# Performance work log

Measured on AMD Instinct MI355X. Metric: run time of the kernel, lower is better.

Reference implementation:

```python
import jax, jax.numpy as jnp
import numpy as np

L = 32768      # sequence length
D_MODEL = 256  # input/output feature dim
D_HIDDEN = 256 # diagonal recurrent state dim
R_MIN, R_MAX, MAX_PHASE = 0.0, 1.0, 6.28


def setup_inputs() -> dict:
    key = jax.random.key(0)
    ks = jax.random.split(key, 8)
    inputs = jax.random.normal(ks[0], (L, D_MODEL), dtype=jnp.float32)
    # nu_init: log(-0.5*log(u*(r_max^2-r_min^2)+r_min^2))
    u1 = jax.random.uniform(ks[1], (D_HIDDEN,), dtype=jnp.float32)
    nu_log = jnp.log(-0.5 * jnp.log(u1 * (R_MAX**2 - R_MIN**2) + R_MIN**2))
    # theta_init: log(max_phase*u)
    u2 = jax.random.uniform(ks[2], (D_HIDDEN,), dtype=jnp.float32)
    theta_log = jnp.log(MAX_PHASE * u2)
    # gamma_log_init from (nu_log, theta_log)
    diag_lambda = jnp.exp(-jnp.exp(nu_log) + 1j * jnp.exp(theta_log))
    gamma_log = jnp.log(jnp.sqrt(1.0 - jnp.abs(diag_lambda) ** 2))
    bnorm = np.sqrt(2 * D_MODEL).astype(np.float32) if False else jnp.sqrt(2.0 * D_MODEL)
    cnorm = jnp.sqrt(2.0 * D_HIDDEN)
    B_re = jax.random.normal(ks[3], (D_HIDDEN, D_MODEL), dtype=jnp.float32) / bnorm
    B_im = jax.random.normal(ks[4], (D_HIDDEN, D_MODEL), dtype=jnp.float32) / bnorm
    C_re = jax.random.normal(ks[5], (D_MODEL, D_HIDDEN), dtype=jnp.float32) / cnorm
    C_im = jax.random.normal(ks[6], (D_MODEL, D_HIDDEN), dtype=jnp.float32) / cnorm
    D = jax.random.normal(ks[7], (D_MODEL,), dtype=jnp.float32)
    return {"inputs": inputs, "nu_log": nu_log, "theta_log": theta_log,
            "gamma_log": gamma_log, "B_re": B_re, "B_im": B_im,
            "C_re": C_re, "C_im": C_im, "D": D}


def _binop(q_i, q_j):
    # elementwise diagonal linear-recurrence combine
    A_i, b_i = q_i
    A_j, b_j = q_j
    return (A_j * A_i, A_j * b_i + b_j)


def reference(inputs, nu_log, theta_log, gamma_log, B_re, B_im, C_re, C_im, D):
    # h_{t+1} = lambda * h_t + B_norm x_{t+1};  y_t = Re[C h_t] + D * x_t
    diag_lambda = jnp.exp(-jnp.exp(nu_log) + 1j * jnp.exp(theta_log))  # (H,)
    B_norm = (B_re + 1j * B_im) * jnp.exp(gamma_log)[:, None]          # (H, M)
    C = C_re + 1j * C_im                                               # (M, H)
    Bu = inputs.astype(B_norm.dtype) @ B_norm.T                        # (L, H) complex
    Lam = jnp.broadcast_to(diag_lambda, (inputs.shape[0], diag_lambda.shape[0]))
    _, h = jax.lax.associative_scan(_binop, (Lam, Bu))                 # (L, H)
    return jnp.real(h @ C.T) + inputs * D                              # (L, M)
```

## Files before the change

### kernel.cpp

```cpp
#include <hip/hip_runtime.h>
#include <hip/hip_bf16.h>
#include <math.h>

#define LSEQ 32768
#define DMODEL 256
#define DHID 256
#define NCH 512
#define CHUNK 128
#define NCHUNKS (LSEQ / CHUNK)

typedef __bf16 bf16_t;
typedef _Float16 f16_t;
typedef __bf16 bf16x8 __attribute__((ext_vector_type(8)));
typedef __bf16 bf16x4 __attribute__((ext_vector_type(4)));
typedef float f32x4 __attribute__((ext_vector_type(4)));

__device__ __forceinline__ void async_load16(const void* g, void* l) {
  __builtin_amdgcn_global_load_lds((__attribute__((address_space(1))) void*)g,
                                   (__attribute__((address_space(3))) void*)l,
                                   16, 0, 0);
}

__device__ __forceinline__ float f16tof(unsigned int u) {
  return (float)__builtin_bit_cast(_Float16, (unsigned short)(u & 0xffffu));
}
__device__ __forceinline__ unsigned short fTobf(float f) {
  return __builtin_bit_cast(unsigned short, (bf16_t)f);
}

__global__ void prep_params(const float* __restrict__ nu_log,
                            const float* __restrict__ theta_log,
                            float* __restrict__ lam ) {
  int h = threadIdx.x;
  if (h < DHID) {
    double nu = exp((double)nu_log[h]);
    double th = exp((double)theta_log[h]);
    double mag = exp(-nu);
    lam[h]            = (float)(mag * cos(th));
    lam[DHID + h]     = (float)(mag * sin(th));
    double magC = exp(-(double)CHUNK * nu);
    double phC  = fmod((double)CHUNK * th, 6.283185307179586);
    lam[2 * DHID + h] = (float)(magC * cos(phC));
    lam[3 * DHID + h] = (float)(magC * sin(phC));
    double mag32 = exp(-32.0 * nu);
    double ph32  = fmod(32.0 * th, 6.283185307179586);
    lam[4 * DHID + h] = (float)(mag32 * cos(ph32));
    lam[5 * DHID + h] = (float)(mag32 * sin(ph32));
  }
}

__global__ void pack_w1(const float* __restrict__ B_re, const float* __restrict__ B_im,
                        const float* __restrict__ gamma_log, bf16_t* __restrict__ W1) {
  int n = blockIdx.x, k = threadIdx.x;
  int h = n >> 1;
  float g = expf(gamma_log[h]);
  float v = (((n & 1) == 0) ? B_re[h * DMODEL + k] : B_im[h * DMODEL + k]) * g;
  W1[n * DMODEL + k] = (bf16_t)v;
}

__global__ void pack_w2(const float* __restrict__ C_re, const float* __restrict__ C_im,
                        bf16_t* __restrict__ W2) {
  int m = blockIdx.x, k = threadIdx.x;
  int h = k >> 1;
  float v = ((k & 1) == 0) ? C_re[m * DHID + h] : -C_im[m * DHID + h];
  W2[m * NCH + k] = (bf16_t)v;
}

__global__ void convert_x(const float* __restrict__ x, bf16_t* __restrict__ xb) {
  int i = blockIdx.x * 256 + threadIdx.x;
  float4 v = ((const float4*)x)[i];
  bf16x4 o = {(bf16_t)v.x, (bf16_t)v.y, (bf16_t)v.z, (bf16_t)v.w};
  ((bf16x4*)xb)[i] = o;
}

__global__ __launch_bounds__(512) void gemm1_scan(
    const bf16_t* __restrict__ A, const bf16_t* __restrict__ Bw,
    f16_t* __restrict__ Bu, const float* __restrict__ lam,
    float* __restrict__ E) {
  __shared__ __align__(16) char smem[69632];
  bf16_t* As = (bf16_t*)smem;
  bf16_t* Bs = (bf16_t*)(smem + 8192);
  char*   Bt = smem;
  float*  Ep = (float*)(smem + 65536);

  const int tid = threadIdx.x;
  const int gx = blockIdx.x;
  const int c  = blockIdx.y;
  const int r0 = c * CHUNK;
  const int c0 = gx * 256;
  const int wave = tid >> 6, lane = tid & 63;
  const int wm = wave & 1, wn = wave >> 1;
  const int lrow = lane & 15, lk = lane >> 4;
  const int ra = tid >> 2, ka = (tid & 3) * 8;

  f32x4 acc[4][4] = {};

  for (int k0 = 0; k0 < DMODEL; k0 += 32) {
    __syncthreads();
    async_load16(A + (size_t)(r0 + ra) * DMODEL + k0 + ka, (char*)As + tid * 16);
    async_load16(Bw + (size_t)(c0 + ra) * DMODEL + k0 + ka, (char*)Bs + tid * 16);
    async_load16(Bw + (size_t)(c0 + 128 + ra) * DMODEL + k0 + ka,
                 (char*)Bs + 8192 + tid * 16);
    __syncthreads();
    bf16x8 af[4], bfr[4];
#pragma unroll
    for (int i = 0; i < 4; ++i)
      af[i] = *(const bf16x8*)(As + (wm * 64 + i * 16 + lrow) * 32 + lk * 8);
#pragma unroll
    for (int j = 0; j < 4; ++j)
      bfr[j] = *(const bf16x8*)(Bs + (wn * 64 + j * 16 + lrow) * 32 + lk * 8);
#pragma unroll
    for (int i = 0; i < 4; ++i)
#pragma unroll
      for (int j = 0; j < 4; ++j)
        acc[i][j] = __builtin_amdgcn_mfma_f32_16x16x32_bf16(af[i], bfr[j], acc[i][j], 0, 0, 0);
  }
  __syncthreads();

#pragma unroll
  for (int i = 0; i < 4; ++i)
#pragma unroll
    for (int r = 0; r < 4; ++r) {
      int row = wm * 64 + i * 16 + lk * 4 + r;
      int key = (row & 7) << 4;
#pragma unroll
      for (int j = 0; j < 4; ++j) {
        int col = wn * 64 + j * 16 + lrow;
        *(f16_t*)(Bt + row * 512 + ((col * 2) ^ key)) = (f16_t)acc[i][j][r];
      }
    }
  __syncthreads();

  char* dst = (char*)Bu + (size_t)r0 * 1024 + gx * 512;
#pragma unroll
  for (int it = 0; it < 8; ++it) {
    int idx = it * 512 + tid;
    int row = idx >> 5, off = (idx & 31) * 16;
    *(f32x4*)(dst + (size_t)row * 1024 + off) = *(const f32x4*)(Bt + row * 512 + off);
  }

  {
    int p = tid & 127, seg = tid >> 7;
    int h = gx * 128 + p;
    float lre = lam[h], lim = lam[DHID + h];
    float sre = 0.f, sim = 0.f;
    int cb = 4 * p;
#pragma unroll 4
    for (int t = 0; t < 32; ++t) {
      int row = seg * 32 + t;
      unsigned int w = *(const unsigned int*)(Bt + row * 512 + (cb ^ ((row & 7) << 4)));
      float bre = f16tof(w), bim = f16tof(w >> 16);
      float nre = fmaf(lre, sre, fmaf(-lim, sim, bre));
      float nim = fmaf(lre, sim, fmaf(lim, sre, bim));
      sre = nre; sim = nim;
    }
    Ep[seg * 256 + 2 * p]     = sre;
    Ep[seg * 256 + 2 * p + 1] = sim;
  }
  __syncthreads();
  if (tid < 128) {
    int p = tid, h = gx * 128 + p;
    float ar = lam[4 * DHID + h], ai = lam[5 * DHID + h];
    float er = Ep[2 * p], ei = Ep[2 * p + 1];
#pragma unroll
    for (int s = 1; s < 4; ++s) {
      float tr = fmaf(ar, er, fmaf(-ai, ei, Ep[s * 256 + 2 * p]));
      float ti = fmaf(ar, ei, fmaf(ai, er, Ep[s * 256 + 2 * p + 1]));
      er = tr; ei = ti;
    }
    E[c * NCH + h]       = er;
    E[c * NCH + 256 + h] = ei;
  }
}

__global__ void scan_pass2(const float* __restrict__ E, const float* __restrict__ lam,
                           float* __restrict__ Sc) {
  int h = blockIdx.x, c = threadIdx.x;
  __shared__ float Ar[NCHUNKS], Ai[NCHUNKS], br[NCHUNKS], bi[NCHUNKS];
  float aR = lam[2 * DHID + h], aI = lam[3 * DHID + h];
  float bR = E[c * NCH + h], bI = E[c * NCH + 256 + h];
  Ar[c] = aR; Ai[c] = aI; br[c] = bR; bi[c] = bI;
  __syncthreads();
  for (int off = 1; off < NCHUNKS; off <<= 1) {
    float paR = 0, paI = 0, pbR = 0, pbI = 0;
    bool has = (c >= off);
    if (has) { paR = Ar[c - off]; paI = Ai[c - off]; pbR = br[c - off]; pbI = bi[c - off]; }
    __syncthreads();
    if (has) {
      float nAR = aR * paR - aI * paI;
      float nAI = aR * paI + aI * paR;
      float nbR = aR * pbR - aI * pbI + bR;
      float nbI = aR * pbI + aI * pbR + bI;
      aR = nAR; aI = nAI; bR = nbR; bI = nbI;
      Ar[c] = aR; Ai[c] = aI; br[c] = bR; bi[c] = bI;
    }
    __syncthreads();
  }
  float inR = (c > 0) ? br[c - 1] : 0.f;
  float inI = (c > 0) ? bi[c - 1] : 0.f;
  Sc[c * NCH + h]       = inR;
  Sc[c * NCH + 256 + h] = inI;
}

__global__ __launch_bounds__(512) void scan_gemm2(
    const f16_t* __restrict__ Bu, const bf16_t* __restrict__ W2,
    const float* __restrict__ lam, const float* __restrict__ Sc,
    const float* __restrict__ X, const float* __restrict__ Dv,
    float* __restrict__ out) {
  __shared__ __align__(16) char smem[147456];
  char*   H  = smem;
  bf16_t* Bs = (bf16_t*)(smem + 131072);
  const int tid = threadIdx.x;
  const int c = blockIdx.x;
  const int wave = tid >> 6, lane = tid & 63;
  const int wm = wave & 1, wn = wave >> 1;
  const int lrow = lane & 15, lk = lane >> 4;
  const int ra = tid >> 2, ka = (tid & 3) * 8;

  const char* src = (const char*)Bu + (size_t)c * CHUNK * 1024;
#pragma unroll
  for (int it = 0; it < 16; ++it)
    async_load16(src + it * 8192 + tid * 16, H + it * 8192 + tid * 16);
  __syncthreads();

  if (tid < 256) {
    int h = tid;
    float lre = lam[h], lim = lam[DHID + h];
    float sre = Sc[c * NCH + h], sim = Sc[c * NCH + 256 + h];
    int cb = 4 * h;
#pragma unroll 4
    for (int t = 0; t < CHUNK; ++t) {
      unsigned int* p = (unsigned int*)(H + t * 1024 + (cb ^ ((t & 7) << 4)));
      unsigned int w = *p;
      float bre = f16tof(w), bim = f16tof(w >> 16);
      float nre = fmaf(lre, sre, fmaf(-lim, sim, bre));
      float nim = fmaf(lre, sim, fmaf(lim, sre, bim));
      sre = nre; sim = nim;
      *p = ((unsigned int)fTobf(sim) << 16) | (unsigned int)fTobf(sre);
    }
  }

  f32x4 acc[4][4] = {};
  for (int k0 = 0; k0 < NCH; k0 += 32) {
    __syncthreads();
    async_load16(W2 + (size_t)ra * NCH + k0 + ka, (char*)Bs + tid * 16);
    async_load16(W2 + (size_t)(128 + ra) * NCH + k0 + ka, (char*)Bs + 8192 + tid * 16);
    __syncthreads();
    bf16x8 af[4], bfr[4];
#pragma unroll
    for (int i = 0; i < 4; ++i) {
      int m = wm * 64 + i * 16 + lrow;
      af[i] = *(const bf16x8*)(H + m * 1024 + ((2 * k0 + lk * 16) ^ ((m & 7) << 4)));
    }
#pragma unroll
    for (int j = 0; j < 4; ++j)
      bfr[j] = *(const bf16x8*)(Bs + (wn * 64 + j * 16 + lrow) * 32 + lk * 8);
#pragma unroll
    for (int i = 0; i < 4; ++i)
#pragma unroll
      for (int j = 0; j < 4; ++j)
        acc[i][j] = __builtin_amdgcn_mfma_f32_16x16x32_bf16(af[i], bfr[j], acc[i][j], 0, 0, 0);
  }

#pragma unroll
  for (int i = 0; i < 4; ++i)
#pragma unroll
    for (int r = 0; r < 4; ++r) {
      int row = c * CHUNK + wm * 64 + i * 16 + lk * 4 + r;
#pragma unroll
      for (int j = 0; j < 4; ++j) {
        int col = wn * 64 + j * 16 + lrow;
        float v = acc[i][j][r] + X[(size_t)row * DMODEL + col] * Dv[col];
        out[(size_t)row * DMODEL + col] = v;
      }
    }
}

extern "C" void kernel_launch(void* const* d_in, const int* in_sizes, int n_in,
                              void* d_out, int out_size, void* d_ws, size_t ws_size,
                              hipStream_t stream) {
  const float* inputs    = (const float*)d_in[0];
  const float* nu_log    = (const float*)d_in[1];
  const float* theta_log = (const float*)d_in[2];
  const float* gamma_log = (const float*)d_in[3];
  const float* B_re      = (const float*)d_in[4];
  const float* B_im      = (const float*)d_in[5];
  const float* C_re      = (const float*)d_in[6];
  const float* C_im      = (const float*)d_in[7];
  const float* Dvec      = (const float*)d_in[8];
  float* out = (float*)d_out;

  char* w = (char*)d_ws;
  bf16_t* W1 = (bf16_t*)w; w += (size_t)NCH * DMODEL * 2;
  bf16_t* W2 = (bf16_t*)w; w += (size_t)DMODEL * NCH * 2;
  float* lam = (float*)w;  w += 8192;
  bf16_t* xb = (bf16_t*)w; w += (size_t)LSEQ * DMODEL * 2;
  f16_t* Bu  = (f16_t*)w;  w += (size_t)LSEQ * NCH * 2;
  float* E   = (float*)w;  w += (size_t)NCHUNKS * NCH * 4;
  float* Sc  = (float*)w;  w += (size_t)NCHUNKS * NCH * 4;

  prep_params<<<1, 256, 0, stream>>>(nu_log, theta_log, lam);
  pack_w1<<<NCH, DMODEL, 0, stream>>>(B_re, B_im, gamma_log, W1);
  pack_w2<<<DMODEL, NCH, 0, stream>>>(C_re, C_im, W2);
  convert_x<<<(LSEQ * DMODEL) / 4 / 256, 256, 0, stream>>>(inputs, xb);

  gemm1_scan<<<dim3(2, NCHUNKS), 512, 0, stream>>>(xb, W1, Bu, lam, E);
  scan_pass2<<<DHID, NCHUNKS, 0, stream>>>(E, lam, Sc);
  scan_gemm2<<<NCHUNKS, 512, 0, stream>>>(Bu, W2, lam, Sc, inputs, Dvec, out);
}
```

Baseline: 165.7 us.

## Fuse GEMM1, chunk scan and GEMM2 into one cooperative kernel with grid sync

Merges the three main kernels into a single cooperative kernel with one block per chunk. The Bu tile stays in shared memory between GEMM1 and GEMM2, which removes the global Bu round trip and the separate scan_pass2 launch. After a grid-wide sync, each block computes its incoming carry serially from the per-chunk end states, combining two halves with precomputed powers of lambda. The costs are serial carry loops of up to 256 steps per block, a grid barrier, and a large shared-memory footprint that needs all 256 blocks to be co-resident.

```diff
diff --git a/kernel.cpp b/kernel.cpp
--- a/kernel.cpp
+++ b/kernel.cpp
@@ -1,4 +1,5 @@
 #include <hip/hip_runtime.h>
+#include <hip/hip_cooperative_groups.h>
 #include <hip/hip_bf16.h>
 #include <math.h>
 
@@ -9,6 +10,8 @@
 #define CHUNK 128
 #define NCHUNKS (LSEQ / CHUNK)
 
+namespace cg = cooperative_groups;
+
 typedef __bf16 bf16_t;
 typedef _Float16 f16_t;
 typedef __bf16 bf16x8 __attribute__((ext_vector_type(8)));
@@ -24,29 +27,27 @@
 __device__ __forceinline__ float f16tof(unsigned int u) {
   return (float)__builtin_bit_cast(_Float16, (unsigned short)(u & 0xffffu));
 }
-__device__ __forceinline__ unsigned short fTobf(float f) {
-  return __builtin_bit_cast(unsigned short, (bf16_t)f);
+__device__ __forceinline__ unsigned int fTobf(float f) {
+  return (unsigned int)__builtin_bit_cast(unsigned short, (bf16_t)f);
 }
 
 __global__ void prep_params(const float* __restrict__ nu_log,
                             const float* __restrict__ theta_log,
-                            float* __restrict__ lam ) {
+                            float* __restrict__ lam) {
   int h = threadIdx.x;
-  if (h < DHID) {
-    double nu = exp((double)nu_log[h]);
-    double th = exp((double)theta_log[h]);
-    double mag = exp(-nu);
-    lam[h]            = (float)(mag * cos(th));
-    lam[DHID + h]     = (float)(mag * sin(th));
-    double magC = exp(-(double)CHUNK * nu);
-    double phC  = fmod((double)CHUNK * th, 6.283185307179586);
-    lam[2 * DHID + h] = (float)(magC * cos(phC));
-    lam[3 * DHID + h] = (float)(magC * sin(phC));
-    double mag32 = exp(-32.0 * nu);
-    double ph32  = fmod(32.0 * th, 6.283185307179586);
-    lam[4 * DHID + h] = (float)(mag32 * cos(ph32));
-    lam[5 * DHID + h] = (float)(mag32 * sin(ph32));
-  }
+  if (h >= DHID) return;
+  double nu = exp((double)nu_log[h]);
+  double th = exp((double)theta_log[h]);
+#define PUT(row, n) { \
+    double mag = exp(-(double)(n) * nu); \
+    double ph  = fmod((double)(n) * th, 6.283185307179586); \
+    lam[(row) * DHID + h]     = (float)(mag * cos(ph)); \
+    lam[((row)+1) * DHID + h] = (float)(mag * sin(ph)); }
+  PUT(0, 1.0)
+  PUT(2, 128.0)
+  PUT(4, 64.0)
+  for (int j = 0; j < 8; ++j) PUT(6 + 2 * j, 128.0 * (double)(1 << j))
+#undef PUT
 }
 
 __global__ void pack_w1(const float* __restrict__ B_re, const float* __restrict__ B_im,
@@ -73,46 +74,51 @@
   ((bf16x4*)xb)[i] = o;
 }
 
-__global__ __launch_bounds__(512) void gemm1_scan(
-    const bf16_t* __restrict__ A, const bf16_t* __restrict__ Bw,
-    f16_t* __restrict__ Bu, const float* __restrict__ lam,
-    float* __restrict__ E) {
-  __shared__ __align__(16) char smem[69632];
-  bf16_t* As = (bf16_t*)smem;
-  bf16_t* Bs = (bf16_t*)(smem + 8192);
-  char*   Bt = smem;
-  float*  Ep = (float*)(smem + 65536);
+__global__ __launch_bounds__(512, 2) void lru_fused(
+    const bf16_t* __restrict__ A,
+    const bf16_t* __restrict__ W1,
+    const bf16_t* __restrict__ W2,
+    const float* __restrict__ lam,
+    float* __restrict__ E,
+    const float* __restrict__ X, const float* __restrict__ Dv,
+    float* __restrict__ out) {
+  __shared__ __align__(16) char smem[151552];
+  char*   H   = smem;
+  bf16_t* As  = (bf16_t*)smem;
+  bf16_t* Bs  = (bf16_t*)(smem + 8192);
+  bf16_t* Bs2 = (bf16_t*)(smem + 131072);
+  float*  Ep  = (float*)(smem + 147456);
 
   const int tid = threadIdx.x;
-  const int gx = blockIdx.x;
-  const int c  = blockIdx.y;
+  const int c = blockIdx.x;
   const int r0 = c * CHUNK;
-  const int c0 = gx * 256;
   const int wave = tid >> 6, lane = tid & 63;
   const int wm = wave & 1, wn = wave >> 1;
   const int lrow = lane & 15, lk = lane >> 4;
-  const int ra = tid >> 2, ka = (tid & 3) * 8;
-
-  f32x4 acc[4][4] = {};
-
+
+  f32x4 acc[4][8] = {};
   for (int k0 = 0; k0 < DMODEL; k0 += 32) {
     __syncthreads();
-    async_load16(A + (size_t)(r0 + ra) * DMODEL + k0 + ka, (char*)As + tid * 16);
-    async_load16(Bw + (size_t)(c0 + ra) * DMODEL + k0 + ka, (char*)Bs + tid * 16);
-    async_load16(Bw + (size_t)(c0 + 128 + ra) * DMODEL + k0 + ka,
-                 (char*)Bs + 8192 + tid * 16);
-    __syncthreads();
-    bf16x8 af[4], bfr[4];
+    async_load16(A + (size_t)(r0 + (tid >> 2)) * DMODEL + k0 + (tid & 3) * 8,
+                 (char*)As + tid * 16);
+#pragma unroll
+    for (int it = 0; it < 4; ++it) {
+      int idx = it * 512 + tid;
+      async_load16(W1 + (size_t)(idx >> 2) * DMODEL + k0 + (idx & 3) * 8,
+                   (char*)Bs + idx * 16);
+    }
+    __syncthreads();
+    bf16x8 af[4], bfr[8];
 #pragma unroll
     for (int i = 0; i < 4; ++i)
       af[i] = *(const bf16x8*)(As + (wm * 64 + i * 16 + lrow) * 32 + lk * 8);
 #pragma unroll
-    for (int j = 0; j < 4; ++j)
-      bfr[j] = *(const bf16x8*)(Bs + (wn * 64 + j * 16 + lrow) * 32 + lk * 8);
+    for (int j = 0; j < 8; ++j)
+      bfr[j] = *(const bf16x8*)(Bs + (wn * 128 + j * 16 + lrow) * 32 + lk * 8);
 #pragma unroll
     for (int i = 0; i < 4; ++i)
 #pragma unroll
-      for (int j = 0; j < 4; ++j)
+      for (int j = 0; j < 8; ++j)
         acc[i][j] = __builtin_amdgcn_mfma_f32_16x16x32_bf16(af[i], bfr[j], acc[i][j], 0, 0, 0);
   }
   __syncthreads();
@@ -124,153 +130,135 @@
       int row = wm * 64 + i * 16 + lk * 4 + r;
       int key = (row & 7) << 4;
 #pragma unroll
-      for (int j = 0; j < 4; ++j) {
-        int col = wn * 64 + j * 16 + lrow;
-        *(f16_t*)(Bt + row * 512 + ((col * 2) ^ key)) = (f16_t)acc[i][j][r];
+      for (int j = 0; j < 8; ++j) {
+        int col = wn * 128 + j * 16 + lrow;
+        *(f16_t*)(H + row * 1024 + ((col * 2) ^ key)) = (f16_t)acc[i][j][r];
       }
     }
   __syncthreads();
 
-  char* dst = (char*)Bu + (size_t)r0 * 1024 + gx * 512;
-#pragma unroll
-  for (int it = 0; it < 8; ++it) {
-    int idx = it * 512 + tid;
-    int row = idx >> 5, off = (idx & 31) * 16;
-    *(f32x4*)(dst + (size_t)row * 1024 + off) = *(const f32x4*)(Bt + row * 512 + off);
-  }
-
   {
-    int p = tid & 127, seg = tid >> 7;
-    int h = gx * 128 + p;
-    float lre = lam[h], lim = lam[DHID + h];
+    int p = tid & 255, seg = tid >> 8;
+    float lre = lam[p], lim = lam[DHID + p];
     float sre = 0.f, sim = 0.f;
     int cb = 4 * p;
 #pragma unroll 4
-    for (int t = 0; t < 32; ++t) {
-      int row = seg * 32 + t;
-      unsigned int w = *(const unsigned int*)(Bt + row * 512 + (cb ^ ((row & 7) << 4)));
+    for (int t = 0; t < 64; ++t) {
+      int row = seg * 64 + t;
+      unsigned int w = *(const unsigned int*)(H + row * 1024 + (cb ^ ((row & 7) << 4)));
       float bre = f16tof(w), bim = f16tof(w >> 16);
       float nre = fmaf(lre, sre, fmaf(-lim, sim, bre));
       float nim = fmaf(lre, sim, fmaf(lim, sre, bim));
       sre = nre; sim = nim;
     }
-    Ep[seg * 256 + 2 * p]     = sre;
-    Ep[seg * 256 + 2 * p + 1] = sim;
-  }
-  __syncthreads();
-  if (tid < 128) {
-    int p = tid, h = gx * 128 + p;
-    float ar = lam[4 * DHID + h], ai = lam[5 * DHID + h];
-    float er = Ep[2 * p], ei = Ep[2 * p + 1];
-#pragma unroll
-    for (int s = 1; s < 4; ++s) {
-      float tr = fmaf(ar, er, fmaf(-ai, ei, Ep[s * 256 + 2 * p]));
-      float ti = fmaf(ar, ei, fmaf(ai, er, Ep[s * 256 + 2 * p + 1]));
-      er = tr; ei = ti;
-    }
-    E[c * NCH + h]       = er;
-    E[c * NCH + 256 + h] = ei;
-  }
-}
-
-__global__ void scan_pass2(const float* __restrict__ E, const float* __restrict__ lam,
-                           float* __restrict__ Sc) {
-  int h = blockIdx.x, c = threadIdx.x;
-  __shared__ float Ar[NCHUNKS], Ai[NCHUNKS], br[NCHUNKS], bi[NCHUNKS];
-  float aR = lam[2 * DHID + h], aI = lam[3 * DHID + h];
-  float bR = E[c * NCH + h], bI = E[c * NCH + 256 + h];
-  Ar[c] = aR; Ai[c] = aI; br[c] = bR; bi[c] = bI;
-  __syncthreads();
-  for (int off = 1; off < NCHUNKS; off <<= 1) {
-    float paR = 0, paI = 0, pbR = 0, pbI = 0;
-    bool has = (c >= off);
-    if (has) { paR = Ar[c - off]; paI = Ai[c - off]; pbR = br[c - off]; pbI = bi[c - off]; }
-    __syncthreads();
-    if (has) {
-      float nAR = aR * paR - aI * paI;
-      float nAI = aR * paI + aI * paR;
-      float nbR = aR * pbR - aI * pbI + bR;
-      float nbI = aR * pbI + aI * pbR + bI;
-      aR = nAR; aI = nAI; bR = nbR; bI = nbI;
-      Ar[c] = aR; Ai[c] = aI; br[c] = bR; bi[c] = bI;
-    }
-    __syncthreads();
-  }
-  float inR = (c > 0) ? br[c - 1] : 0.f;
-  float inI = (c > 0) ? bi[c - 1] : 0.f;
-  Sc[c * NCH + h]       = inR;
-  Sc[c * NCH + 256 + h] = inI;
-}
-
-__global__ __launch_bounds__(512) void scan_gemm2(
-    const f16_t* __restrict__ Bu, const bf16_t* __restrict__ W2,
-    const float* __restrict__ lam, const float* __restrict__ Sc,
-    const float* __restrict__ X, const float* __restrict__ Dv,
-    float* __restrict__ out) {
-  __shared__ __align__(16) char smem[147456];
-  char*   H  = smem;
-  bf16_t* Bs = (bf16_t*)(smem + 131072);
-  const int tid = threadIdx.x;
-  const int c = blockIdx.x;
-  const int wave = tid >> 6, lane = tid & 63;
-  const int wm = wave & 1, wn = wave >> 1;
-  const int lrow = lane & 15, lk = lane >> 4;
-  const int ra = tid >> 2, ka = (tid & 3) * 8;
-
-  const char* src = (const char*)Bu + (size_t)c * CHUNK * 1024;
-#pragma unroll
-  for (int it = 0; it < 16; ++it)
-    async_load16(src + it * 8192 + tid * 16, H + it * 8192 + tid * 16);
-  __syncthreads();
-
+    Ep[seg * 512 + 2 * p]     = sre;
+    Ep[seg * 512 + 2 * p + 1] = sim;
+  }
+  __syncthreads();
   if (tid < 256) {
-    int h = tid;
-    float lre = lam[h], lim = lam[DHID + h];
-    float sre = Sc[c * NCH + h], sim = Sc[c * NCH + 256 + h];
-    int cb = 4 * h;
+    int p = tid;
+    float ar = lam[4 * DHID + p], ai = lam[5 * DHID + p];
+    float s0r = Ep[2 * p], s0i = Ep[2 * p + 1];
+    float s1r = Ep[512 + 2 * p], s1i = Ep[512 + 2 * p + 1];
+    float er = fmaf(ar, s0r, fmaf(-ai, s0i, s1r));
+    float ei = fmaf(ar, s0i, fmaf(ai, s0r, s1i));
+    E[(size_t)c * NCH + 2 * p]     = er;
+    E[(size_t)c * NCH + 2 * p + 1] = ei;
+  }
+  __threadfence();
+  cg::this_grid().sync();
+  __threadfence();
+
+  float carR = 0.f, carI = 0.f;
+  {
+    int p = tid & 255, hi = tid >> 8;
+    int half = c >> 1;
+    int lo = hi ? half : 0;
+    int hiEnd = hi ? c : half;
+    float aR = lam[2 * DHID + p], aI = lam[3 * DHID + p];
+    float sr = 0.f, si = 0.f;
+#pragma unroll 4
+    for (int k = lo; k < hiEnd; ++k) {
+      float2 e = *(const float2*)(E + (size_t)k * NCH + 2 * p);
+      float nr = fmaf(aR, sr, fmaf(-aI, si, e.x));
+      float ni = fmaf(aR, si, fmaf(aI, sr, e.y));
+      sr = nr; si = ni;
+    }
+    Ep[hi * 512 + 2 * p]     = sr;
+    Ep[hi * 512 + 2 * p + 1] = si;
+  }
+  __syncthreads();
+  if (tid < 256) {
+    int p = tid;
+    int lenb = c - (c >> 1);
+    float pr = 1.f, pi = 0.f;
+#pragma unroll
+    for (int j = 0; j < 8; ++j)
+      if (lenb & (1 << j)) {
+        float br = lam[(6 + 2 * j) * DHID + p], bi = lam[(7 + 2 * j) * DHID + p];
+        float nr = pr * br - pi * bi;
+        float ni = pr * bi + pi * br;
+        pr = nr; pi = ni;
+      }
+    float sar = Ep[2 * p], sai = Ep[2 * p + 1];
+    float sbr = Ep[512 + 2 * p], sbi = Ep[512 + 2 * p + 1];
+    carR = fmaf(pr, sar, fmaf(-pi, sai, sbr));
+    carI = fmaf(pr, sai, fmaf(pi, sar, sbi));
+  }
+  __syncthreads();
+
+  if (tid < 256) {
+    int p = tid;
+    float lre = lam[p], lim = lam[DHID + p];
+    float sre = carR, sim = carI;
+    int cb = 4 * p;
 #pragma unroll 4
     for (int t = 0; t < CHUNK; ++t) {
-      unsigned int* p = (unsigned int*)(H + t * 1024 + (cb ^ ((t & 7) << 4)));
-      unsigned int w = *p;
+      unsigned int* ptr = (unsigned int*)(H + t * 1024 + (cb ^ ((t & 7) << 4)));
+      unsigned int w = *ptr;
       float bre = f16tof(w), bim = f16tof(w >> 16);
       float nre = fmaf(lre, sre, fmaf(-lim, sim, bre));
       float nim = fmaf(lre, sim, fmaf(lim, sre, bim));
       sre = nre; sim = nim;
-      *p = ((unsigned int)fTobf(sim) << 16) | (unsigned int)fTobf(sre);
-    }
-  }
-
-  f32x4 acc[4][4] = {};
+      *ptr = (fTobf(sim) << 16) | fTobf(sre);
+    }
+  }
+
+  f32x4 acc2[4][4] = {};
   for (int k0 = 0; k0 < NCH; k0 += 32) {
     __syncthreads();
-    async_load16(W2 + (size_t)ra * NCH + k0 + ka, (char*)Bs + tid * 16);
-    async_load16(W2 + (size_t)(128 + ra) * NCH + k0 + ka, (char*)Bs + 8192 + tid * 16);
-    __syncthreads();
-    bf16x8 af[4], bfr[4];
+#pragma unroll
+    for (int it = 0; it < 2; ++it) {
+      int idx = it * 512 + tid;
+      async_load16(W2 + (size_t)(idx >> 2) * NCH + k0 + (idx & 3) * 8,
+                   (char*)Bs2 + idx * 16);
+    }
+    __syncthreads();
+    bf16x8 af2[4], bf2[4];
 #pragma unroll
     for (int i = 0; i < 4; ++i) {
       int m = wm * 64 + i * 16 + lrow;
-      af[i] = *(const bf16x8*)(H + m * 1024 + ((2 * k0 + lk * 16) ^ ((m & 7) << 4)));
+      af2[i] = *(const bf16x8*)(H + m * 1024 + ((2 * k0 + lk * 16) ^ ((m & 7) << 4)));
     }
 #pragma unroll
     for (int j = 0; j < 4; ++j)
-      bfr[j] = *(const bf16x8*)(Bs + (wn * 64 + j * 16 + lrow) * 32 + lk * 8);
+      bf2[j] = *(const bf16x8*)(Bs2 + (wn * 64 + j * 16 + lrow) * 32 + lk * 8);
 #pragma unroll
     for (int i = 0; i < 4; ++i)
 #pragma unroll
       for (int j = 0; j < 4; ++j)
-        acc[i][j] = __builtin_amdgcn_mfma_f32_16x16x32_bf16(af[i], bfr[j], acc[i][j], 0, 0, 0);
+        acc2[i][j] = __builtin_amdgcn_mfma_f32_16x16x32_bf16(af2[i], bf2[j], acc2[i][j], 0, 0, 0);
   }
 
 #pragma unroll
   for (int i = 0; i < 4; ++i)
 #pragma unroll
     for (int r = 0; r < 4; ++r) {
-      int row = c * CHUNK + wm * 64 + i * 16 + lk * 4 + r;
+      int row = r0 + wm * 64 + i * 16 + lk * 4 + r;
 #pragma unroll
       for (int j = 0; j < 4; ++j) {
         int col = wn * 64 + j * 16 + lrow;
-        float v = acc[i][j][r] + X[(size_t)row * DMODEL + col] * Dv[col];
+        float v = acc2[i][j][r] + X[(size_t)row * DMODEL + col] * Dv[col];
         out[(size_t)row * DMODEL + col] = v;
       }
     }
@@ -293,18 +281,16 @@
   char* w = (char*)d_ws;
   bf16_t* W1 = (bf16_t*)w; w += (size_t)NCH * DMODEL * 2;
   bf16_t* W2 = (bf16_t*)w; w += (size_t)DMODEL * NCH * 2;
-  float* lam = (float*)w;  w += 8192;
+  float* lam = (float*)w;  w += 24576;
   bf16_t* xb = (bf16_t*)w; w += (size_t)LSEQ * DMODEL * 2;
-  f16_t* Bu  = (f16_t*)w;  w += (size_t)LSEQ * NCH * 2;
   float* E   = (float*)w;  w += (size_t)NCHUNKS * NCH * 4;
-  float* Sc  = (float*)w;  w += (size_t)NCHUNKS * NCH * 4;
 
   prep_params<<<1, 256, 0, stream>>>(nu_log, theta_log, lam);
   pack_w1<<<NCH, DMODEL, 0, stream>>>(B_re, B_im, gamma_log, W1);
   pack_w2<<<DMODEL, NCH, 0, stream>>>(C_re, C_im, W2);
   convert_x<<<(LSEQ * DMODEL) / 4 / 256, 256, 0, stream>>>(inputs, xb);
 
-  gemm1_scan<<<dim3(2, NCHUNKS), 512, 0, stream>>>(xb, W1, Bu, lam, E);
-  scan_pass2<<<DHID, NCHUNKS, 0, stream>>>(E, lam, Sc);
-  scan_gemm2<<<NCHUNKS, 512, 0, stream>>>(Bu, W2, lam, Sc, inputs, Dvec, out);
-}
+  void* args[] = {&xb, &W1, &W2, &lam, &E, &inputs, &Dvec, &out};
+  hipLaunchCooperativeKernel((const void*)lru_fused, dim3(NCHUNKS), dim3(512),
+                             args, 0, stream);
+}
```

New measurement: 290.5 us. +75.3%, slower.

## Fuse prep kernels and fold cross-chunk carry scan into scan_gemm2

Applied to the files above, without the earlier changes.

Merges the four preprocessing kernels into one launch. It also drops the separate scan_pass2 kernel: each scan_gemm2 block now recomputes its own incoming state by sequentially combining all previous chunk end-states, split into two halves that are joined with precomputed powers of lambda. Blocks are issued in reverse chunk order to balance the O(c) carry loop. This removes two launches and an intermediate buffer, at the cost of redundant quadratic work over chunk summaries (up to 256 serial steps per block).

```diff
diff --git a/kernel.cpp b/kernel.cpp
--- a/kernel.cpp
+++ b/kernel.cpp
@@ -24,53 +24,50 @@
 __device__ __forceinline__ float f16tof(unsigned int u) {
   return (float)__builtin_bit_cast(_Float16, (unsigned short)(u & 0xffffu));
 }
-__device__ __forceinline__ unsigned short fTobf(float f) {
-  return __builtin_bit_cast(unsigned short, (bf16_t)f);
-}
-
-__global__ void prep_params(const float* __restrict__ nu_log,
-                            const float* __restrict__ theta_log,
-                            float* __restrict__ lam ) {
-  int h = threadIdx.x;
-  if (h < DHID) {
-    double nu = exp((double)nu_log[h]);
-    double th = exp((double)theta_log[h]);
-    double mag = exp(-nu);
-    lam[h]            = (float)(mag * cos(th));
-    lam[DHID + h]     = (float)(mag * sin(th));
-    double magC = exp(-(double)CHUNK * nu);
-    double phC  = fmod((double)CHUNK * th, 6.283185307179586);
-    lam[2 * DHID + h] = (float)(magC * cos(phC));
-    lam[3 * DHID + h] = (float)(magC * sin(phC));
-    double mag32 = exp(-32.0 * nu);
-    double ph32  = fmod(32.0 * th, 6.283185307179586);
-    lam[4 * DHID + h] = (float)(mag32 * cos(ph32));
-    lam[5 * DHID + h] = (float)(mag32 * sin(ph32));
-  }
-}
-
-__global__ void pack_w1(const float* __restrict__ B_re, const float* __restrict__ B_im,
-                        const float* __restrict__ gamma_log, bf16_t* __restrict__ W1) {
-  int n = blockIdx.x, k = threadIdx.x;
-  int h = n >> 1;
-  float g = expf(gamma_log[h]);
-  float v = (((n & 1) == 0) ? B_re[h * DMODEL + k] : B_im[h * DMODEL + k]) * g;
-  W1[n * DMODEL + k] = (bf16_t)v;
-}
-
-__global__ void pack_w2(const float* __restrict__ C_re, const float* __restrict__ C_im,
-                        bf16_t* __restrict__ W2) {
-  int m = blockIdx.x, k = threadIdx.x;
-  int h = k >> 1;
-  float v = ((k & 1) == 0) ? C_re[m * DHID + h] : -C_im[m * DHID + h];
-  W2[m * NCH + k] = (bf16_t)v;
-}
-
-__global__ void convert_x(const float* __restrict__ x, bf16_t* __restrict__ xb) {
-  int i = blockIdx.x * 256 + threadIdx.x;
-  float4 v = ((const float4*)x)[i];
-  bf16x4 o = {(bf16_t)v.x, (bf16_t)v.y, (bf16_t)v.z, (bf16_t)v.w};
-  ((bf16x4*)xb)[i] = o;
+__device__ __forceinline__ unsigned int fTobf(float f) {
+  return (unsigned int)__builtin_bit_cast(unsigned short, (bf16_t)f);
+}
+
+__global__ void prep_all(const float* __restrict__ nu_log,
+                         const float* __restrict__ theta_log,
+                         const float* __restrict__ gamma_log,
+                         const float* __restrict__ B_re, const float* __restrict__ B_im,
+                         const float* __restrict__ C_re, const float* __restrict__ C_im,
+                         const float* __restrict__ x,
+                         float* __restrict__ lam, bf16_t* __restrict__ W1,
+                         bf16_t* __restrict__ W2, bf16_t* __restrict__ xb) {
+  const int bid = blockIdx.x, tid = threadIdx.x;
+  if (bid == 0) {
+    int h = tid;
+    if (h < DHID) {
+      double nu = exp((double)nu_log[h]);
+      double th = exp((double)theta_log[h]);
+#define PUT(row, n) { \
+      double mag = exp(-(double)(n) * nu); \
+      double ph  = fmod((double)(n) * th, 6.283185307179586); \
+      lam[(row) * DHID + h]     = (float)(mag * cos(ph)); \
+      lam[((row)+1) * DHID + h] = (float)(mag * sin(ph)); }
+      PUT(0, 1.0)
+      PUT(2, 32.0)
+      for (int j = 0; j < 8; ++j) PUT(4 + 2 * j, 128.0 * (double)(1 << j))
+#undef PUT
+    }
+  } else if (bid < 513) {
+    int n = bid - 1, k = tid, h = n >> 1;
+    float g = expf(gamma_log[h]);
+    float v = (((n & 1) == 0) ? B_re[h * DMODEL + k] : B_im[h * DMODEL + k]) * g;
+    W1[n * DMODEL + k] = (bf16_t)v;
+  } else if (bid < 1025) {
+    int idx = bid - 513;
+    int m = idx >> 1, k = (idx & 1) * 256 + tid, h = k >> 1;
+    float v = ((k & 1) == 0) ? C_re[m * DHID + h] : -C_im[m * DHID + h];
+    W2[m * NCH + k] = (bf16_t)v;
+  } else {
+    int i = (bid - 1025) * 256 + tid;
+    float4 v = ((const float4*)x)[i];
+    bf16x4 o = {(bf16_t)v.x, (bf16_t)v.y, (bf16_t)v.z, (bf16_t)v.w};
+    ((bf16x4*)xb)[i] = o;
+  }
 }
 
 __global__ __launch_bounds__(512) void gemm1_scan(
@@ -160,7 +157,7 @@
   __syncthreads();
   if (tid < 128) {
     int p = tid, h = gx * 128 + p;
-    float ar = lam[4 * DHID + h], ai = lam[5 * DHID + h];
+    float ar = lam[2 * DHID + h], ai = lam[3 * DHID + h];
     float er = Ep[2 * p], ei = Ep[2 * p + 1];
 #pragma unroll
     for (int s = 1; s < 4; ++s) {
@@ -168,83 +165,92 @@
       float ti = fmaf(ar, ei, fmaf(ai, er, Ep[s * 256 + 2 * p + 1]));
       er = tr; ei = ti;
     }
-    E[c * NCH + h]       = er;
-    E[c * NCH + 256 + h] = ei;
-  }
-}
-
-__global__ void scan_pass2(const float* __restrict__ E, const float* __restrict__ lam,
-                           float* __restrict__ Sc) {
-  int h = blockIdx.x, c = threadIdx.x;
-  __shared__ float Ar[NCHUNKS], Ai[NCHUNKS], br[NCHUNKS], bi[NCHUNKS];
-  float aR = lam[2 * DHID + h], aI = lam[3 * DHID + h];
-  float bR = E[c * NCH + h], bI = E[c * NCH + 256 + h];
-  Ar[c] = aR; Ai[c] = aI; br[c] = bR; bi[c] = bI;
-  __syncthreads();
-  for (int off = 1; off < NCHUNKS; off <<= 1) {
-    float paR = 0, paI = 0, pbR = 0, pbI = 0;
-    bool has = (c >= off);
-    if (has) { paR = Ar[c - off]; paI = Ai[c - off]; pbR = br[c - off]; pbI = bi[c - off]; }
-    __syncthreads();
-    if (has) {
-      float nAR = aR * paR - aI * paI;
-      float nAI = aR * paI + aI * paR;
-      float nbR = aR * pbR - aI * pbI + bR;
-      float nbI = aR * pbI + aI * pbR + bI;
-      aR = nAR; aI = nAI; bR = nbR; bI = nbI;
-      Ar[c] = aR; Ai[c] = aI; br[c] = bR; bi[c] = bI;
-    }
-    __syncthreads();
-  }
-  float inR = (c > 0) ? br[c - 1] : 0.f;
-  float inI = (c > 0) ? bi[c - 1] : 0.f;
-  Sc[c * NCH + h]       = inR;
-  Sc[c * NCH + 256 + h] = inI;
+    E[(size_t)c * NCH + 2 * h]     = er;
+    E[(size_t)c * NCH + 2 * h + 1] = ei;
+  }
 }
 
 __global__ __launch_bounds__(512) void scan_gemm2(
     const f16_t* __restrict__ Bu, const bf16_t* __restrict__ W2,
-    const float* __restrict__ lam, const float* __restrict__ Sc,
+    const float* __restrict__ lam, const float* __restrict__ E,
     const float* __restrict__ X, const float* __restrict__ Dv,
     float* __restrict__ out) {
   __shared__ __align__(16) char smem[147456];
   char*   H  = smem;
   bf16_t* Bs = (bf16_t*)(smem + 131072);
+  float*  Ep = (float*)(smem + 131072);
+
   const int tid = threadIdx.x;
-  const int c = blockIdx.x;
+  const int c = (int)gridDim.x - 1 - (int)blockIdx.x;
+  const int r0 = c * CHUNK;
+
+  const char* src = (const char*)Bu + (size_t)r0 * 1024;
+#pragma unroll
+  for (int it = 0; it < 16; ++it)
+    async_load16(src + it * 8192 + tid * 16, H + it * 8192 + tid * 16);
+
+  {
+    int p = tid & 255, half = tid >> 8;
+    int m = c >> 1;
+    int lo = half ? m : 0, end = half ? c : m;
+    float aR = lam[4 * DHID + p], aI = lam[5 * DHID + p];
+    float sr = 0.f, si = 0.f;
+#pragma unroll 4
+    for (int k = lo; k < end; ++k) {
+      float2 e = *(const float2*)(E + (size_t)k * NCH + 2 * p);
+      float nr = fmaf(aR, sr, fmaf(-aI, si, e.x));
+      float ni = fmaf(aR, si, fmaf(aI, sr, e.y));
+      sr = nr; si = ni;
+    }
+    Ep[half * 512 + 2 * p]     = sr;
+    Ep[half * 512 + 2 * p + 1] = si;
+  }
+  __syncthreads();
+
+  if (tid < 256) {
+    int p = tid;
+    int lenb = c - (c >> 1);
+    float pr = 1.f, pi = 0.f;
+#pragma unroll
+    for (int j = 0; j < 8; ++j)
+      if (lenb & (1 << j)) {
+        float br = lam[(4 + 2 * j) * DHID + p], bi = lam[(5 + 2 * j) * DHID + p];
+        float nr = pr * br - pi * bi, ni = pr * bi + pi * br;
+        pr = nr; pi = ni;
+      }
+    float sar = Ep[2 * p], sai = Ep[2 * p + 1];
+    float sbr = Ep[512 + 2 * p], sbi = Ep[512 + 2 * p + 1];
+    float carR = fmaf(pr, sar, fmaf(-pi, sai, sbr));
+    float carI = fmaf(pr, sai, fmaf(pi, sar, sbi));
+
+    float lre = lam[p], lim = lam[DHID + p];
+    float sre = carR, sim = carI;
+    int cb = 4 * p;
+#pragma unroll 4
+    for (int t = 0; t < CHUNK; ++t) {
+      unsigned int* ptr = (unsigned int*)(H + t * 1024 + (cb ^ ((t & 7) << 4)));
+      unsigned int w = *ptr;
+      float bre = f16tof(w), bim = f16tof(w >> 16);
+      float nre = fmaf(lre, sre, fmaf(-lim, sim, bre));
+      float nim = fmaf(lre, sim, fmaf(lim, sre, bim));
+      sre = nre; sim = nim;
+      *ptr = (fTobf(sim) << 16) | fTobf(sre);
+    }
+  }
+
   const int wave = tid >> 6, lane = tid & 63;
   const int wm = wave & 1, wn = wave >> 1;
   const int lrow = lane & 15, lk = lane >> 4;
   const int ra = tid >> 2, ka = (tid & 3) * 8;
-
-  const char* src = (const char*)Bu + (size_t)c * CHUNK * 1024;
-#pragma unroll
-  for (int it = 0; it < 16; ++it)
-    async_load16(src + it * 8192 + tid * 16, H + it * 8192 + tid * 16);
-  __syncthreads();
-
-  if (tid < 256) {
-    int h = tid;
-    float lre = lam[h], lim = lam[DHID + h];
-    float sre = Sc[c * NCH + h], sim = Sc[c * NCH + 256 + h];
-    int cb = 4 * h;
-#pragma unroll 4
-    for (int t = 0; t < CHUNK; ++t) {
-      unsigned int* p = (unsigned int*)(H + t * 1024 + (cb ^ ((t & 7) << 4)));
-      unsigned int w = *p;
-      float bre = f16tof(w), bim = f16tof(w >> 16);
-      float nre = fmaf(lre, sre, fmaf(-lim, sim, bre));
-      float nim = fmaf(lre, sim, fmaf(lim, sre, bim));
-      sre = nre; sim = nim;
-      *p = ((unsigned int)fTobf(sim) << 16) | (unsigned int)fTobf(sre);
-    }
-  }
-
   f32x4 acc[4][4] = {};
   for (int k0 = 0; k0 < NCH; k0 += 32) {
     __syncthreads();
-    async_load16(W2 + (size_t)ra * NCH + k0 + ka, (char*)Bs + tid * 16);
-    async_load16(W2 + (size_t)(128 + ra) * NCH + k0 + ka, (char*)Bs + 8192 + tid * 16);
+#pragma unroll
+    for (int it = 0; it < 2; ++it) {
+      int idx = it * 512 + tid;
+      async_load16(W2 + (size_t)(idx >> 2) * NCH + k0 + (idx & 3) * 8,
+                   (char*)Bs + idx * 16);
+    }
     __syncthreads();
     bf16x8 af[4], bfr[4];
 #pragma unroll
@@ -266,7 +272,7 @@
   for (int i = 0; i < 4; ++i)
 #pragma unroll
     for (int r = 0; r < 4; ++r) {
-      int row = c * CHUNK + wm * 64 + i * 16 + lk * 4 + r;
+      int row = r0 + wm * 64 + i * 16 + lk * 4 + r;
 #pragma unroll
       for (int j = 0; j < 4; ++j) {
         int col = wn * 64 + j * 16 + lrow;
@@ -293,18 +299,14 @@
   char* w = (char*)d_ws;
   bf16_t* W1 = (bf16_t*)w; w += (size_t)NCH * DMODEL * 2;
   bf16_t* W2 = (bf16_t*)w; w += (size_t)DMODEL * NCH * 2;
-  float* lam = (float*)w;  w += 8192;
+  float* lam = (float*)w;  w += 24576;
   bf16_t* xb = (bf16_t*)w; w += (size_t)LSEQ * DMODEL * 2;
   f16_t* Bu  = (f16_t*)w;  w += (size_t)LSEQ * NCH * 2;
   float* E   = (float*)w;  w += (size_t)NCHUNKS * NCH * 4;
-  float* Sc  = (float*)w;  w += (size_t)NCHUNKS * NCH * 4;
-
-  prep_params<<<1, 256, 0, stream>>>(nu_log, theta_log, lam);
-  pack_w1<<<NCH, DMODEL, 0, stream>>>(B_re, B_im, gamma_log, W1);
-  pack_w2<<<DMODEL, NCH, 0, stream>>>(C_re, C_im, W2);
-  convert_x<<<(LSEQ * DMODEL) / 4 / 256, 256, 0, stream>>>(inputs, xb);
-
+
+  prep_all<<<9217, 256, 0, stream>>>(nu_log, theta_log, gamma_log,
+                                     B_re, B_im, C_re, C_im, inputs,
+                                     lam, W1, W2, xb);
   gemm1_scan<<<dim3(2, NCHUNKS), 512, 0, stream>>>(xb, W1, Bu, lam, E);
-  scan_pass2<<<DHID, NCHUNKS, 0, stream>>>(E, lam, Sc);
-  scan_gemm2<<<NCHUNKS, 512, 0, stream>>>(Bu, W2, lam, Sc, inputs, Dvec, out);
-}
+  scan_gemm2<<<NCHUNKS, 512, 0, stream>>>(Bu, W2, lam, E, inputs, Dvec, out);
+}
```

New measurement: 157.1 us. -5.2%, faster.
